# Optimization experiments

Measured on AMD Instinct MI355X. Metric: run time of the kernel, lower is better.

## Reference

```python
import jax, jax.numpy as jnp
import numpy as np

DIM = 1536
NH = 12
HD = DIM // NH  # 128
FF, HH, WW = 32, 8, 12
L = FF * HH * WW  # 3072
WIN = (8, 4, 4)  # block of 128 tokens
BLK = WIN[0] * WIN[1] * WIN[2]


def rms_norm(x, g, eps=1e-5):
    # matches RMSNorm: normalize in fp32, scale by weight
    v = jnp.mean(jnp.square(x), axis=-1, keepdims=True)
    return x * jax.lax.rsqrt(v + eps) * g


def rope(x, freqs, n):
    # x: [B,S,D]; freqs: [S,1,HD/2,2] (cos,sin); complex rotation on pairs
    B, S, D = x.shape
    xr = x.reshape(B, S, n, D // n // 2, 2)
    c, s = freqs[..., 0], freqs[..., 1]        # [S,1,HD/2] broadcast over B,n
    a, b = xr[..., 0], xr[..., 1]
    out = jnp.stack([a * c - b * s, a * s + b * c], axis=-1)
    return out.reshape(B, S, D)


def partition3d(x, f, h, w):
    # [B,f,h,w,D] -> [B, nblocks, 128, D], block order (f/8, h/4, w/4)
    B, D = x.shape[0], x.shape[-1]
    wf, wh, ww = WIN
    x = x.reshape(B, f // wf, wf, h // wh, wh, w // ww, ww, D)
    x = x.transpose(0, 1, 3, 5, 2, 4, 6, 7)
    return x.reshape(B, -1, BLK, D)


def reverse3d(xw, f, h, w):
    # [B, nblocks, 128, D] -> [B, f*h*w, D]
    B, D = xw.shape[0], xw.shape[-1]
    wf, wh, ww = WIN
    x = xw.reshape(B, f // wf, h // wh, w // ww, wf, wh, ww, D)
    x = x.transpose(0, 1, 4, 2, 5, 3, 6, 7)
    return x.reshape(B, f * h * w, D)


def block_mask(f, h, w):
    # build_local_block_mask_3d: spatial mask is all-ones; temporal = context|local
    seqlen = f // WIN[0]
    nb_sp = (h // WIN[1]) * (w // WIN[2])
    stride = WIN[0]
    ctx_idx = (6 + stride - 1) // stride - 1          # context_frames=6
    radius = (5 + stride - 1) // stride               # temp_window_frames=5
    t = jnp.arange(seqlen)
    mt = (t[None, :] <= ctx_idx) | (jnp.abs(t[:, None] - t[None, :]) <= radius)
    # expand temporal block mask over spatial blocks -> [nb, nb]
    return jnp.repeat(jnp.repeat(mt, nb_sp, axis=0), nb_sp, axis=1)


def setup_inputs() -> dict:
    key = jax.random.key(0)
    ks = jax.random.split(key, 8)
    x = jax.random.normal(ks[0], (1, L, DIM), jnp.float32)
    ang = jax.random.uniform(ks[1], (L, 1, HD // 2), jnp.float32, 0.0, 2.0 * np.pi)
    freqs = jnp.stack([jnp.cos(ang), jnp.sin(ang)], axis=-1)  # [L,1,64,2]
    sc = 1.0 / np.sqrt(DIM)
    Wq = jax.random.normal(ks[2], (DIM, DIM), jnp.float32) * sc
    Wk = jax.random.normal(ks[3], (DIM, DIM), jnp.float32) * sc
    Wv = jax.random.normal(ks[4], (DIM, DIM), jnp.float32) * sc
    Wo = jax.random.normal(ks[5], (DIM, DIM), jnp.float32) * sc
    zeros = jnp.zeros((DIM,), jnp.float32)
    ones = jnp.ones((DIM,), jnp.float32)
    return {"x": x, "freqs": freqs, "Wq": Wq, "bq": zeros, "Wk": Wk, "bk": zeros,
            "Wv": Wv, "bv": zeros, "Wo": Wo, "bo": zeros, "g_q": ones, "g_k": ones,
            "f": FF, "h": HH, "w": WW, "local_range": 18}


def reference(x, freqs, Wq, bq, Wk, bk, Wv, bv, Wo, bo, g_q, g_k, f, h, w, local_range):
    B, S, D = x.shape
    q = rms_norm(x @ Wq + bq, g_q, eps=1e-5)
    k = rms_norm(x @ Wk + bk, g_k, eps=1e-5)
    v = x @ Wv + bv
    q = rope(q, freqs, NH)
    k = rope(k, freqs, NH)
    # window partition and flatten back to a reordered sequence
    qs = partition3d(q.reshape(B, f, h, w, D), f, h, w).reshape(B, S, D)
    ks_ = partition3d(k.reshape(B, f, h, w, D), f, h, w).reshape(B, S, D)
    vs = partition3d(v.reshape(B, f, h, w, D), f, h, w).reshape(B, S, D)
    bm = block_mask(f, h, w)                       # [nb, nb] bool
    tok_mask = jnp.repeat(jnp.repeat(bm, BLK, 0), BLK, 1)  # [S, S]
    qh = qs.reshape(B, S, NH, HD).transpose(0, 2, 1, 3)
    kh = ks_.reshape(B, S, NH, HD).transpose(0, 2, 1, 3)
    vh = vs.reshape(B, S, NH, HD).transpose(0, 2, 1, 3)
    scores = jnp.einsum('bhqd,bhkd->bhqk', qh, kh) / np.sqrt(HD)
    scores = jnp.where(tok_mask[None, None], scores, -jnp.inf)
    attn = jax.nn.softmax(scores, axis=-1)
    out = jnp.einsum('bhqk,bhkd->bhqd', attn, vh)
    out = out.transpose(0, 2, 1, 3).reshape(B, S, D)
    out = reverse3d(out.reshape(B, -1, BLK, D), f, h, w)  # undo window reorder
    return out @ Wo + bo
```

## Files before the change

### kernel.cpp

```cpp
#include <hip/hip_runtime.h>
#include <hip/hip_bf16.h>
#include <math.h>

#define S_LEN 3072
#define DMODEL 1536
#define NQKV 4608
#define NHEAD 12
#define HDIM 128
#define NSPLIT 4

typedef __attribute__((ext_vector_type(8))) short bf16x8;
typedef __attribute__((ext_vector_type(4))) float f32x4;
typedef __attribute__((ext_vector_type(4))) unsigned int u32x4;

__device__ __forceinline__ void gload_lds16(const void* g, void* lds) {
  __builtin_amdgcn_global_load_lds(
      (const __attribute__((address_space(1))) unsigned int*)g,
      (__attribute__((address_space(3))) unsigned int*)lds, 16, 0, 0);
}

__device__ __forceinline__ int invperm(int p) {
  int blk = p >> 7;
  int w   = p & 127;
  int fb  = blk / 6;
  int rem = blk - fb * 6;
  int hb  = rem / 3;
  int wb  = rem - hb * 3;
  int fi  = fb * 8 + (w >> 4);
  int hi  = hb * 4 + ((w >> 2) & 3);
  int wi  = wb * 4 + (w & 3);
  return (fi * 8 + hi) * 12 + wi;
}

__device__ __forceinline__ int fwdperm(int s) {
  int fi = s / 96;
  int rem = s - fi * 96;
  int hi = rem / 12;
  int wi = rem - hi * 12;
  int fb = fi >> 3, wf = fi & 7;
  int hb = hi >> 2, wh = hi & 3;
  int wb = wi >> 2, ww = wi & 3;
  return ((fb * 2 + hb) * 3 + wb) * 128 + wf * 16 + wh * 4 + ww;
}

__device__ __forceinline__ void store_out(float* p, float v) { *p = v; }
__device__ __forceinline__ void store_out(__hip_bfloat16* p, float v) { *p = __float2bfloat16(v); }

__global__ __launch_bounds__(256) void convert_bias(
    const float* __restrict__ in, __hip_bfloat16* __restrict__ out,
    const float* __restrict__ bq, const float* __restrict__ bk,
    const float* __restrict__ bv, float* __restrict__ bqkv)
{
  if (blockIdx.x < 4608) {
    int i = blockIdx.x * 256 + threadIdx.x;
    float4 v = ((const float4*)in)[i];
    __hip_bfloat16 b[4] = {__float2bfloat16(v.x), __float2bfloat16(v.y),
                           __float2bfloat16(v.z), __float2bfloat16(v.w)};
    ((ushort4*)out)[i] = *(ushort4*)b;
  } else {
    int j = (blockIdx.x - 4608) * 256 + threadIdx.x;
    float v = (j < 1536) ? bq[j] : (j < 3072) ? bk[j - 1536] : bv[j - 3072];
    bqkv[j] = v;
  }
}

__global__ __launch_bounds__(256) void transpose_convert4(
    const float* __restrict__ W0, const float* __restrict__ W1,
    const float* __restrict__ W2, const float* __restrict__ W3,
    __hip_bfloat16* __restrict__ Wtqkv, __hip_bfloat16* __restrict__ Wot)
{
  __shared__ __hip_bfloat16 Ls[64][67];
  const int z = blockIdx.z;
  const float* W = (z == 0) ? W0 : (z == 1) ? W1 : (z == 2) ? W2 : W3;
  __hip_bfloat16* Wt = (z < 3) ? Wtqkv + (size_t)z * DMODEL * DMODEL : Wot;
  const int r0 = blockIdx.y * 64, c0 = blockIdx.x * 64, t = threadIdx.x;
  {
    int rr = t >> 2, cb = (t & 3) * 16;
    const float4* src = (const float4*)(W + (size_t)(r0 + rr) * DMODEL + c0 + cb);
    #pragma unroll
    for (int i = 0; i < 4; ++i) {
      float4 v = src[i];
      Ls[rr][cb + i * 4 + 0] = __float2bfloat16(v.x);
      Ls[rr][cb + i * 4 + 1] = __float2bfloat16(v.y);
      Ls[rr][cb + i * 4 + 2] = __float2bfloat16(v.z);
      Ls[rr][cb + i * 4 + 3] = __float2bfloat16(v.w);
    }
  }
  __syncthreads();
  {
    int cc = t >> 2, rb = (t & 3) * 16;
    unsigned short tmp[16];
    #pragma unroll
    for (int i = 0; i < 16; ++i) tmp[i] = *(unsigned short*)&Ls[rb + i][cc];
    uint4* dst = (uint4*)(Wt + (size_t)(c0 + cc) * DMODEL + r0 + rb);
    dst[0] = ((uint4*)tmp)[0];
    dst[1] = ((uint4*)tmp)[1];
  }
}

template <typename OutT, int BN>
__global__ __launch_bounds__(256) void gemm_bt(
    const __hip_bfloat16* __restrict__ A, const __hip_bfloat16* __restrict__ Bt,
    const float* __restrict__ bias, OutT* __restrict__ C, int M, int N, int K)
{
  constexpr int NB = BN / 32;
  __shared__ __hip_bfloat16 As[2][128 * 32];
  __shared__ __hip_bfloat16 Bs[2][BN * 32];
  const int tid = threadIdx.x, lane = tid & 63, wid = tid >> 6;
  const int l15 = lane & 15, l4 = lane >> 4;
  const int nwg = gridDim.x * gridDim.y;
  const int lin = blockIdx.y * gridDim.x + blockIdx.x;
  const int cpx = nwg >> 3;
  const int swz = (lin & 7) * cpx + (lin >> 3);
  const int row0 = (swz / gridDim.x) * 128, col0 = (swz % gridDim.x) * BN;
  const int wr = (wid >> 1) * 64, wc = (wid & 1) * (BN / 2);

  f32x4 acc[4][NB] = {};
  const char* Ab = (const char*)A;
  const char* Bb = (const char*)Bt;

  auto STAGE = [&](int buf, int k0) {
    #pragma unroll
    for (int i = 0; i < 2; ++i) {
      int slot = i * 256 + tid;
      int r = slot >> 2;
      int b = (slot & 3) * 16;
      gload_lds16(Ab + ((size_t)(row0 + r) * K + k0) * 2 + b,
                  (char*)As[buf] + ((size_t)i * 256 + wid * 64) * 16);
    }
    #pragma unroll
    for (int i = 0; i < BN / 64; ++i) {
      int slot = i * 256 + tid;
      int r = slot >> 2;
      int b = (slot & 3) * 16;
      gload_lds16(Bb + ((size_t)(col0 + r) * K + k0) * 2 + b,
                  (char*)Bs[buf] + ((size_t)i * 256 + wid * 64) * 16);
    }
  };

  STAGE(0, 0);
  __syncthreads();
  int cur = 0;
  for (int k0 = 0; k0 < K; k0 += 32) {
    if (k0 + 32 < K) STAGE(cur ^ 1, k0 + 32);
    bf16x8 a[4], b[NB];
    #pragma unroll
    for (int m = 0; m < 4; ++m)
      a[m] = *(const bf16x8*)&As[cur][(wr + m * 16 + l15) * 32 + l4 * 8];
    #pragma unroll
    for (int n = 0; n < NB; ++n)
      b[n] = *(const bf16x8*)&Bs[cur][(wc + n * 16 + l15) * 32 + l4 * 8];
    #pragma unroll
    for (int m = 0; m < 4; ++m)
      #pragma unroll
      for (int n = 0; n < NB; ++n)
        acc[m][n] = __builtin_amdgcn_mfma_f32_16x16x32_bf16(a[m], b[n], acc[m][n], 0, 0, 0);
    __syncthreads();
    cur ^= 1;
  }

  #pragma unroll
  for (int m = 0; m < 4; ++m) {
    #pragma unroll
    for (int r = 0; r < 4; ++r) {
      size_t row = row0 + wr + m * 16 + l4 * 4 + r;
      #pragma unroll
      for (int n = 0; n < NB; ++n) {
        int col = col0 + wc + n * 16 + l15;
        store_out(&C[row * N + col], acc[m][n][r] + bias[col]);
      }
    }
  }
}

__global__ __launch_bounds__(256) void norm_rope_perm(
    const __hip_bfloat16* __restrict__ X,
    const float* __restrict__ gq, const float* __restrict__ gk,
    const float* __restrict__ freqs,
    __hip_bfloat16* __restrict__ OutQ, __hip_bfloat16* __restrict__ OutK)
{
  const int s = blockIdx.x, tid = threadIdx.x;
  const int sec = blockIdx.y;
  const float* g = sec ? gk : gq;
  __hip_bfloat16* Out = sec ? OutK : OutQ;
  const float qsc = sec ? 1.0f : (0.08838834764831843f * 1.4426950408889634f);
  const unsigned int* row = (const unsigned int*)(X + (size_t)s * NQKV + sec * 1536);
  float e0[3], e1[3];
  float ss = 0.f;
  #pragma unroll
  for (int i = 0; i < 3; ++i) {
    unsigned int u = row[tid + i * 256];
    float a = __uint_as_float(u << 16);
    float b = __uint_as_float(u & 0xffff0000u);
    e0[i] = a; e1[i] = b;
    ss += a * a + b * b;
  }
  #pragma unroll
  for (int off = 32; off > 0; off >>= 1) ss += __shfl_down(ss, off, 64);
  __shared__ float wsum[4];
  if ((tid & 63) == 0) wsum[tid >> 6] = ss;
  __syncthreads();
  float rs = rsqrtf((wsum[0] + wsum[1] + wsum[2] + wsum[3]) * (1.f / DMODEL) + 1e-5f);
  rs *= qsc;
  const int p = fwdperm(s);
  #pragma unroll
  for (int i = 0; i < 3; ++i) {
    int pi = tid + i * 256;
    int n = pi >> 6, d2 = pi & 63;
    float c  = freqs[(size_t)s * 128 + 2 * d2];
    float sn = freqs[(size_t)s * 128 + 2 * d2 + 1];
    float y0 = e0[i] * rs * g[2 * pi];
    float y1 = e1[i] * rs * g[2 * pi + 1];
    float o0 = y0 * c - y1 * sn;
    float o1 = y0 * sn + y1 * c;
    __hip_bfloat16 b0 = __float2bfloat16(o0), b1 = __float2bfloat16(o1);
    unsigned int u = ((unsigned int)(*(unsigned short*)&b1) << 16) | (*(unsigned short*)&b0);
    ((unsigned int*)Out)[(((size_t)n * S_LEN + p) * HDIM + 2 * d2) >> 1] = u;
  }
}

__global__ __launch_bounds__(256) void v_transpose(
    const __hip_bfloat16* __restrict__ Vsec, __hip_bfloat16* __restrict__ Vt)
{
  __shared__ __hip_bfloat16 Ls[64][136];
  const int p0 = blockIdx.x * 64, h = blockIdx.y, t = threadIdx.x;
  {
    int pl = t & 63, dg = t >> 6;
    int sidx = invperm(p0 + pl);
    const uint4* src = (const uint4*)(Vsec + (size_t)sidx * NQKV + h * HDIM + dg * 32);
    #pragma unroll
    for (int i = 0; i < 4; ++i) {
      uint4 v = src[i];
      *(uint4*)&Ls[pl][dg * 32 + i * 8] = v;
    }
  }
  __syncthreads();
  {
    int d = t >> 1, ph = t & 1;
    unsigned short tmp[32];
    #pragma unroll
    for (int i = 0; i < 32; ++i) tmp[i] = *(unsigned short*)&Ls[ph * 32 + i][d];
    uint4* dst = (uint4*)(Vt + ((size_t)h * HDIM + d) * S_LEN + p0 + ph * 32);
    #pragma unroll
    for (int i = 0; i < 4; ++i) dst[i] = ((uint4*)tmp)[i];
  }
}

__global__ __launch_bounds__(512) void attn_mfma(
    const __hip_bfloat16* __restrict__ Qp, const __hip_bfloat16* __restrict__ Kp,
    const __hip_bfloat16* __restrict__ Vt,
    __hip_bfloat16* __restrict__ Opart, float* __restrict__ ml)
{
  __shared__ __hip_bfloat16 Ks[64 * 128];
  __shared__ __hip_bfloat16 Vs[128 * 64];

  const int hw = blockIdx.x + 24 * (blockIdx.y + NSPLIT * blockIdx.z);
  const int L  = (hw & 7) * 144 + (hw >> 3);
  const int j  = L % 6;
  const int t4 = (L / 6) & 3;
  const int sh = L / 24;
  const int h  = sh % 12;
  const int split = sh / 12;
  const int tg = (t4 == 0) ? 2 : (t4 == 1) ? 1 : (t4 == 2) ? 3 : 0;
  const int qb = tg * 6 + j;

  const int tid = threadIdx.x, lane = tid & 63, wid = tid >> 6;
  const int l15 = lane & 15, l4 = lane >> 4;

  const int NCh = (tg == 0) ? 6 : (tg == 2) ? 12 : 9;
  const int cbegin = split * NCh, cend = cbegin + NCh;

  const char* Kh = (const char*)(Kp + (size_t)h * S_LEN * HDIM);
  const char* Vh = (const char*)(Vt + (size_t)h * HDIM * S_LEN);

  const int kbase = 8 * (l15 >> 2) + (l15 & 3);
  const int ksw = (((l15 & 3) | (((l15 >> 2) & 1) << 2))) << 4;

  unsigned int koffA, voffA;
  {
    unsigned int kr = tid >> 4;
    unsigned int sig = (kr & 3) | (((kr >> 3) & 1) << 2);
    koffA = kr * 256 + (((tid & 15) * 16) ^ (sig << 4));
    unsigned int vr = tid >> 3;
    voffA = vr * (S_LEN * 2) + (((tid & 7) * 16) ^ ((vr & 7) << 4));
  }

  auto k0_of = [&](int ci) { return ci * 64 + ((tg == 3 && ci >= 12) ? 768 : 0); };
  auto STAGE = [&](int k0) {
    const char* ks = Kh + (size_t)k0 * 256;
    gload_lds16(ks + koffA,        (char*)Ks + tid * 16);
    gload_lds16(ks + koffA + 8192, (char*)Ks + tid * 16 + 8192);
    const char* vs = Vh + (size_t)k0 * 2 + voffA;
    gload_lds16(vs,                          (char*)Vs + tid * 16);
    gload_lds16(vs + (size_t)64 * S_LEN * 2, (char*)Vs + tid * 16 + 8192);
  };

  bf16x8 aq[4];
  {
    const __hip_bfloat16* qr = Qp + (size_t)h * S_LEN * HDIM
        + (size_t)(qb * 128 + wid * 16 + l15) * HDIM + l4 * 8;
    #pragma unroll
    for (int dc = 0; dc < 4; ++dc) aq[dc] = *(const bf16x8*)(qr + dc * 32);
  }

  f32x4 oacc[8] = {};
  float m2 = -1e30f;
  float lsum = 0.f;

  for (int ci = cbegin; ci < cend; ++ci) {
    const int k0 = k0_of(ci);
    STAGE(k0);
    __syncthreads();

    f32x4 sfr[4] = {};
    #pragma unroll
    for (int ct = 0; ct < 4; ++ct) {
      int key = kbase + (ct >> 1) * 32 + (ct & 1) * 4;
      #pragma unroll
      for (int dc = 0; dc < 4; ++dc) {
        int b = (dc * 64 + l4 * 16) ^ ksw;
        bf16x8 kf = *(const bf16x8*)((const char*)Ks + key * 256 + b);
        sfr[ct] = __builtin_amdgcn_mfma_f32_16x16x32_bf16(kf, aq[dc], sfr[ct], 0, 0, 0);
      }
    }
    float lmax = fmaxf(
        fmaxf(fmaxf(sfr[0][0], sfr[0][1]), fmaxf(sfr[0][2], sfr[0][3])),
        fmaxf(fmaxf(fmaxf(sfr[1][0], sfr[1][1]), fmaxf(sfr[1][2], sfr[1][3])),
              fmaxf(fmaxf(fmaxf(sfr[2][0], sfr[2][1]), fmaxf(sfr[2][2], sfr[2][3])),
                    fmaxf(fmaxf(sfr[3][0], sfr[3][1]), fmaxf(sfr[3][2], sfr[3][3])))));
    bool grow = lmax > m2 + 8.f;
    if (ci == cbegin || __any(grow)) {
      float mf = lmax;
      mf = fmaxf(mf, __shfl_xor(mf, 16, 64));
      mf = fmaxf(mf, __shfl_xor(mf, 32, 64));
      float mn = fmaxf(m2, mf);
      float corr = exp2f(m2 - mn);
      m2 = mn;
      lsum *= corr;
      float cr[4];
      #pragma unroll
      for (int r = 0; r < 4; ++r) cr[r] = __shfl(corr, l4 * 4 + r, 64);
      #pragma unroll
      for (int n = 0; n < 8; ++n)
        #pragma unroll
        for (int r = 0; r < 4; ++r) oacc[n][r] *= cr[r];
    }
    #pragma unroll
    for (int ct = 0; ct < 4; ++ct)
      #pragma unroll
      for (int r = 0; r < 4; ++r) {
        float p = exp2f(sfr[ct][r] - m2);
        sfr[ct][r] = p;
        lsum += p;
      }
    #pragma unroll
    for (int ks = 0; ks < 2; ++ks) {
      u32x4 wv;
      {
        __hip_bfloat16 a0 = __float2bfloat16(sfr[2 * ks][0]);
        __hip_bfloat16 a1 = __float2bfloat16(sfr[2 * ks][1]);
        __hip_bfloat16 a2 = __float2bfloat16(sfr[2 * ks][2]);
        __hip_bfloat16 a3 = __float2bfloat16(sfr[2 * ks][3]);
        __hip_bfloat16 b0 = __float2bfloat16(sfr[2 * ks + 1][0]);
        __hip_bfloat16 b1 = __float2bfloat16(sfr[2 * ks + 1][1]);
        __hip_bfloat16 b2 = __float2bfloat16(sfr[2 * ks + 1][2]);
        __hip_bfloat16 b3 = __float2bfloat16(sfr[2 * ks + 1][3]);
        wv[0] = ((unsigned int)(*(unsigned short*)&a1) << 16) | (*(unsigned short*)&a0);
        wv[1] = ((unsigned int)(*(unsigned short*)&a3) << 16) | (*(unsigned short*)&a2);
        wv[2] = ((unsigned int)(*(unsigned short*)&b1) << 16) | (*(unsigned short*)&b0);
        wv[3] = ((unsigned int)(*(unsigned short*)&b3) << 16) | (*(unsigned short*)&b2);
      }
      bf16x8 pa = __builtin_bit_cast(bf16x8, wv);
      #pragma unroll
      for (int n = 0; n < 8; ++n) {
        int d = n * 16 + l15;
        int b = (ks * 64 + l4 * 16) ^ ((d & 7) << 4);
        bf16x8 bv = *(const bf16x8*)((const char*)Vs + d * 128 + b);
        oacc[n] = __builtin_amdgcn_mfma_f32_16x16x32_bf16(pa, bv, oacc[n], 0, 0, 0);
      }
    }
    __syncthreads();
  }

  float t = lsum;
  t += __shfl_xor(t, 16, 64);
  t += __shfl_xor(t, 32, 64);
  float inv = 1.0f / t;
  #pragma unroll
  for (int r = 0; r < 4; ++r) {
    float invr = __shfl(inv, l4 * 4 + r, 64);
    int qrow = qb * 128 + wid * 16 + l4 * 4 + r;
    size_t rowid = (size_t)(split * NHEAD + h) * S_LEN + qrow;
    __hip_bfloat16* dst = Opart + rowid * HDIM;
    #pragma unroll
    for (int n = 0; n < 8; ++n)
      dst[n * 16 + l15] = __float2bfloat16(oacc[n][r] * invr);
  }
  if (lane < 16) {
    int qrow = qb * 128 + wid * 16 + lane;
    size_t rowid = (size_t)(split * NHEAD + h) * S_LEN + qrow;
    ml[rowid * 2 + 0] = m2;
    ml[rowid * 2 + 1] = t;
  }
}

__global__ __launch_bounds__(256) void attn_merge(
    const __hip_bfloat16* __restrict__ Opart, const float* __restrict__ ml,
    __hip_bfloat16* __restrict__ AO)
{
  const int rid = blockIdx.x * 4 + (threadIdx.x >> 6);
  const int lane = threadIdx.x & 63;
  const int h = rid / S_LEN, q = rid - h * S_LEN;
  size_t rr[NSPLIT];
  float m[NSPLIT], l[NSPLIT];
  float mm = -1e30f;
  #pragma unroll
  for (int s = 0; s < NSPLIT; ++s) {
    rr[s] = (size_t)(s * NHEAD + h) * S_LEN + q;
    m[s] = ml[rr[s] * 2];
    l[s] = ml[rr[s] * 2 + 1];
    mm = fmaxf(mm, m[s]);
  }
  float wsum = 0.f, wgt[NSPLIT];
  #pragma unroll
  for (int s = 0; s < NSPLIT; ++s) { wgt[s] = l[s] * exp2f(m[s] - mm); wsum += wgt[s]; }
  float inv = 1.0f / wsum;
  float o0 = 0.f, o1 = 0.f;
  #pragma unroll
  for (int s = 0; s < NSPLIT; ++s) {
    unsigned int u = ((const unsigned int*)(Opart + rr[s] * HDIM))[lane];
    float a = wgt[s] * inv;
    o0 += a * __uint_as_float(u << 16);
    o1 += a * __uint_as_float(u & 0xffff0000u);
  }
  __hip_bfloat16 b0 = __float2bfloat16(o0), b1 = __float2bfloat16(o1);
  unsigned int u = ((unsigned int)(*(unsigned short*)&b1) << 16) | (*(unsigned short*)&b0);
  int sorig = invperm(q);
  ((unsigned int*)(AO + (size_t)sorig * DMODEL + h * HDIM))[lane] = u;
}

extern "C" void kernel_launch(void* const* d_in, const int* in_sizes, int n_in,
                              void* d_out, int out_size, void* d_ws, size_t ws_size,
                              hipStream_t stream)
{
  (void)in_sizes; (void)n_in; (void)out_size; (void)ws_size;
  const float* x     = (const float*)d_in[0];
  const float* freqs = (const float*)d_in[1];
  const float* Wq    = (const float*)d_in[2];
  const float* bq    = (const float*)d_in[3];
  const float* Wk    = (const float*)d_in[4];
  const float* bk    = (const float*)d_in[5];
  const float* Wv    = (const float*)d_in[6];
  const float* bv    = (const float*)d_in[7];
  const float* Wo    = (const float*)d_in[8];
  const float* bo    = (const float*)d_in[9];
  const float* gq    = (const float*)d_in[10];
  const float* gk    = (const float*)d_in[11];
  float* out = (float*)d_out;

  char* w = (char*)d_ws;
  __hip_bfloat16* xbf    = (__hip_bfloat16*)(w);
  __hip_bfloat16* Wtqkv  = (__hip_bfloat16*)(w + 9437184);
  __hip_bfloat16* QKVbf  = (__hip_bfloat16*)(w + 23592960);
  __hip_bfloat16* Qp     = (__hip_bfloat16*)(w + 51904512);
  __hip_bfloat16* Kp     = (__hip_bfloat16*)(w + 61341696);
  __hip_bfloat16* Vtb    = (__hip_bfloat16*)(w + 70778880);
  __hip_bfloat16* AO     = (__hip_bfloat16*)(w + 80216064);
  __hip_bfloat16* Wot    = (__hip_bfloat16*)(w + 89653248);
  float*          bqkv   = (float*)(w + 94371840);
  __hip_bfloat16* Opart  = (__hip_bfloat16*)(w + 9437184);
  float*          mlbuf  = (float*)(w);

  hipLaunchKernelGGL(convert_bias, dim3(4626), dim3(256), 0, stream,
                     x, xbf, bq, bk, bv, bqkv);
  hipLaunchKernelGGL(transpose_convert4, dim3(24, 24, 4), dim3(256), 0, stream,
                     Wq, Wk, Wv, Wo, Wtqkv, Wot);

  hipLaunchKernelGGL((gemm_bt<__hip_bfloat16, 128>), dim3(NQKV / 128, S_LEN / 128),
                     dim3(256), 0, stream, xbf, Wtqkv, bqkv, QKVbf, S_LEN, NQKV, DMODEL);

  hipLaunchKernelGGL(norm_rope_perm, dim3(S_LEN, 2), dim3(256), 0, stream,
                     QKVbf, gq, gk, freqs, Qp, Kp);
  hipLaunchKernelGGL(v_transpose, dim3(48, 12), dim3(256), 0, stream, QKVbf + 3072, Vtb);

  hipLaunchKernelGGL(attn_mfma, dim3(24, NSPLIT, NHEAD), dim3(512), 0, stream,
                     Qp, Kp, Vtb, Opart, mlbuf);
  hipLaunchKernelGGL(attn_merge, dim3(S_LEN * NHEAD / 4), dim3(256), 0, stream,
                     Opart, mlbuf, AO);

  hipLaunchKernelGGL((gemm_bt<float, 64>), dim3(DMODEL / 64, S_LEN / 128),
                     dim3(256), 0, stream, AO, Wot, bo, out, S_LEN, DMODEL, DMODEL);
}
```

Before: 227.9 us.

## Single-buffer GEMM LDS, XCD-grouped tile mapping, and MFMA priority hints in attention

The GEMM drops LDS double buffering and loads each k-step synchronously before compute, which halves LDS use and may raise occupancy but removes the overlap of loads with MFMA work. The block-to-tile swizzle now gives each XCD a contiguous 2D sub-grid of output tiles to improve L2 reuse of A and B. In the attention kernel, s_setprio raises wave priority around the MFMA loops so issue is favored while other waves do softmax work. The remap assumes gridDim.x is divisible by 4 and gridDim.y by 2.

Result: no change. 232.1 us (+1.8%).

```diff
diff --git a/kernel.cpp b/kernel.cpp
--- a/kernel.cpp
+++ b/kernel.cpp
@@ -104,29 +104,30 @@
     const float* __restrict__ bias, OutT* __restrict__ C, int M, int N, int K)
 {
   constexpr int NB = BN / 32;
-  __shared__ __hip_bfloat16 As[2][128 * 32];
-  __shared__ __hip_bfloat16 Bs[2][BN * 32];
+  __shared__ __hip_bfloat16 As[128 * 32];
+  __shared__ __hip_bfloat16 Bs[BN * 32];
   const int tid = threadIdx.x, lane = tid & 63, wid = tid >> 6;
   const int l15 = lane & 15, l4 = lane >> 4;
-  const int nwg = gridDim.x * gridDim.y;
   const int lin = blockIdx.y * gridDim.x + blockIdx.x;
-  const int cpx = nwg >> 3;
-  const int swz = (lin & 7) * cpx + (lin >> 3);
-  const int row0 = (swz / gridDim.x) * 128, col0 = (swz % gridDim.x) * BN;
+  const int xcd = lin & 7, idx = lin >> 3;
+  const int CX = gridDim.x >> 2, CY = gridDim.y >> 1;
+  const int cx = xcd & 3, cy = xcd >> 2;
+  const int lc = idx % CX, lr = idx / CX;
+  const int row0 = (cy * CY + lr) * 128, col0 = (cx * CX + lc) * BN;
   const int wr = (wid >> 1) * 64, wc = (wid & 1) * (BN / 2);
 
   f32x4 acc[4][NB] = {};
   const char* Ab = (const char*)A;
   const char* Bb = (const char*)Bt;
 
-  auto STAGE = [&](int buf, int k0) {
+  auto STAGE = [&](int k0) {
     #pragma unroll
     for (int i = 0; i < 2; ++i) {
       int slot = i * 256 + tid;
       int r = slot >> 2;
       int b = (slot & 3) * 16;
       gload_lds16(Ab + ((size_t)(row0 + r) * K + k0) * 2 + b,
-                  (char*)As[buf] + ((size_t)i * 256 + wid * 64) * 16);
+                  (char*)As + ((size_t)i * 256 + wid * 64) * 16);
     }
     #pragma unroll
     for (int i = 0; i < BN / 64; ++i) {
@@ -134,29 +135,26 @@
       int r = slot >> 2;
       int b = (slot & 3) * 16;
       gload_lds16(Bb + ((size_t)(col0 + r) * K + k0) * 2 + b,
-                  (char*)Bs[buf] + ((size_t)i * 256 + wid * 64) * 16);
+                  (char*)Bs + ((size_t)i * 256 + wid * 64) * 16);
     }
   };
 
-  STAGE(0, 0);
-  __syncthreads();
-  int cur = 0;
   for (int k0 = 0; k0 < K; k0 += 32) {
-    if (k0 + 32 < K) STAGE(cur ^ 1, k0 + 32);
+    STAGE(k0);
+    __syncthreads();
     bf16x8 a[4], b[NB];
     #pragma unroll
     for (int m = 0; m < 4; ++m)
-      a[m] = *(const bf16x8*)&As[cur][(wr + m * 16 + l15) * 32 + l4 * 8];
+      a[m] = *(const bf16x8*)&As[(wr + m * 16 + l15) * 32 + l4 * 8];
     #pragma unroll
     for (int n = 0; n < NB; ++n)
-      b[n] = *(const bf16x8*)&Bs[cur][(wc + n * 16 + l15) * 32 + l4 * 8];
+      b[n] = *(const bf16x8*)&Bs[(wc + n * 16 + l15) * 32 + l4 * 8];
     #pragma unroll
     for (int m = 0; m < 4; ++m)
       #pragma unroll
       for (int n = 0; n < NB; ++n)
         acc[m][n] = __builtin_amdgcn_mfma_f32_16x16x32_bf16(a[m], b[n], acc[m][n], 0, 0, 0);
     __syncthreads();
-    cur ^= 1;
   }
 
   #pragma unroll
@@ -313,6 +311,7 @@
     __syncthreads();
 
     f32x4 sfr[4] = {};
+    __builtin_amdgcn_s_setprio(1);
     #pragma unroll
     for (int ct = 0; ct < 4; ++ct) {
       int key = kbase + (ct >> 1) * 32 + (ct & 1) * 4;
@@ -323,6 +322,7 @@
         sfr[ct] = __builtin_amdgcn_mfma_f32_16x16x32_bf16(kf, aq[dc], sfr[ct], 0, 0, 0);
       }
     }
+    __builtin_amdgcn_s_setprio(0);
     float lmax = fmaxf(
         fmaxf(fmaxf(sfr[0][0], sfr[0][1]), fmaxf(sfr[0][2], sfr[0][3])),
         fmaxf(fmaxf(fmaxf(sfr[1][0], sfr[1][1]), fmaxf(sfr[1][2], sfr[1][3])),
@@ -371,6 +371,7 @@
         wv[3] = ((unsigned int)(*(unsigned short*)&b3) << 16) | (*(unsigned short*)&b2);
       }
       bf16x8 pa = __builtin_bit_cast(bf16x8, wv);
+      __builtin_amdgcn_s_setprio(1);
       #pragma unroll
       for (int n = 0; n < 8; ++n) {
         int d = n * 16 + l15;
@@ -378,6 +379,7 @@
         bf16x8 bv = *(const bf16x8*)((const char*)Vs + d * 128 + b);
         oacc[n] = __builtin_amdgcn_mfma_f32_16x16x32_bf16(pa, bv, oacc[n], 0, 0, 0);
       }
+      __builtin_amdgcn_s_setprio(0);
     }
     __syncthreads();
   }
```
